# Optimization experiments

Hardware: AMD Instinct MI355X
Metric: run time of the kernel (lower is better)

Reference implementation:

```python
import jax, jax.numpy as jnp
import numpy as np

N, K, C, SP = 65536, 16, 64, 8
C8 = C // SP  # attn_nn output dim == C // share_planes == 8
E = N * K
EPS = 1e-5


def _bn(x, g, b):
    # BatchNorm1d in training mode: batch statistics over the row dim
    mu = x.mean(0)
    var = ((x - mu) ** 2).mean(0)
    return (x - mu) * jax.lax.rsqrt(var + EPS) * g + b


def _segment_softmax(a, seg, n):
    m = jax.ops.segment_max(a, seg, num_segments=n)
    e = jnp.exp(a - m[seg])
    s = jax.ops.segment_sum(e, seg, num_segments=n)
    return e / s[seg]


def setup_inputs() -> dict:
    key = jax.random.key(0)
    ks = jax.random.split(key, 12)

    def w(k, shape, fan_in):
        return jax.random.normal(k, shape, jnp.float32) / np.sqrt(fan_in).astype(np.float32)

    x = jax.random.normal(ks[0], (N, C), jnp.float32)
    pos = jax.random.uniform(ks[1], (N, 3), jnp.float32)
    src = jax.random.randint(ks[2], (E,), 0, N)          # knn neighbor ids
    dst = jnp.repeat(jnp.arange(N), K)                   # k neighbors per target node
    edge_index = jnp.stack([src, dst]).astype(jnp.int32)
    return dict(
        x=x, pos=pos, edge_index=edge_index,
        W_in=w(ks[3], (C, C), C), W_out=w(ks[4], (C, C), C),
        pos_w1=w(ks[5], (3, 3), 3), pos_b1=jnp.zeros(3, jnp.float32),
        pos_bn_g=jnp.ones(3, jnp.float32), pos_bn_b=jnp.zeros(3, jnp.float32),
        pos_w2=w(ks[6], (C, 3), 3), pos_b2=jnp.zeros(C, jnp.float32),
        attn_bn1_g=jnp.ones(C, jnp.float32), attn_bn1_b=jnp.zeros(C, jnp.float32),
        attn_w1=w(ks[7], (C8, C), C), attn_b1=jnp.zeros(C8, jnp.float32),
        attn_bn2_g=jnp.ones(C8, jnp.float32), attn_bn2_b=jnp.zeros(C8, jnp.float32),
        attn_w2=w(ks[8], (C8, C8), C8), attn_b2=jnp.zeros(C8, jnp.float32),
        lin_w=w(ks[9], (C, C), C), lin_b=jnp.zeros(C, jnp.float32),
        src_w=w(ks[10], (C, C), C), src_b=jnp.zeros(C, jnp.float32),
        dst_w=w(ks[11], (C, C), C), dst_b=jnp.zeros(C, jnp.float32),
        bn1_g=jnp.ones(C, jnp.float32), bn1_b=jnp.zeros(C, jnp.float32),
        bn2_g=jnp.ones(C, jnp.float32), bn2_b=jnp.zeros(C, jnp.float32),
        bn3_g=jnp.ones(C, jnp.float32), bn3_b=jnp.zeros(C, jnp.float32),
    )


def reference(x, pos, edge_index, W_in, W_out, pos_w1, pos_b1, pos_bn_g, pos_bn_b,
              pos_w2, pos_b2, attn_bn1_g, attn_bn1_b, attn_w1, attn_b1,
              attn_bn2_g, attn_bn2_b, attn_w2, attn_b2, lin_w, lin_b,
              src_w, src_b, dst_w, dst_b, bn1_g, bn1_b, bn2_g, bn2_b, bn3_g, bn3_b):
    src, dst = edge_index[0], edge_index[1]
    x_skip = x
    # lin_in + bn1 + relu
    h = jax.nn.relu(_bn(x @ W_in.T, bn1_g, bn1_b))

    # --- PointTransformerConv ---
    a_src = h @ src_w.T + src_b
    a_dst = h @ dst_w.T + dst_b
    hW = h @ lin_w.T + lin_b

    rel = pos[src] - pos[dst]              # pos_j - pos_i  [E,3]
    d = jax.nn.relu(_bn(rel @ pos_w1.T + pos_b1, pos_bn_g, pos_bn_b))
    delta = d @ pos_w2.T + pos_b2          # [E,C]

    a = a_src[src] - a_dst[dst] + delta    # alpha_j - alpha_i + delta  [E,C]
    # attn_nn: BN -> ReLU -> (Lin C->C8, BN, ReLU) -> Lin C8->C8
    a = jax.nn.relu(_bn(a, attn_bn1_g, attn_bn1_b))
    a = jax.nn.relu(_bn(a @ attn_w1.T + attn_b1, attn_bn2_g, attn_bn2_b))
    a = a @ attn_w2.T + attn_b2            # [E,C8]
    alpha = _segment_softmax(a, dst, N)    # softmax over each node's neighborhood

    # grouped weighting with share_planes: [E,SP,C8] * [E,1,C8]
    msg = (alpha[:, None, :] * (hW[src] + delta).reshape(E, SP, C8)).reshape(E, C)
    out = jax.ops.segment_sum(msg, dst, num_segments=N)  # aggr='add'

    h2 = jax.nn.relu(_bn(out, bn2_g, bn2_b))
    h3 = _bn(h2 @ W_out.T, bn3_g, bn3_b)
    return jax.nn.relu(h3 + x_skip)
```

## Files before the change

kernel.cpp:

```cpp
#include <hip/hip_runtime.h>
#include <cstddef>

constexpr int N_ = 65536;
constexpr int K_ = 16;
constexpr int E_ = N_ * K_;
constexpr int C_ = 64;
#define EPS_ 1e-5f
#define SW 68
#define INV_N (1.f / 65536.f)
#define INV_E (1.f / 1048576.f)
#define NSLOT 64

typedef unsigned int uint_t;
typedef float f32x4_t __attribute__((ext_vector_type(4)));
typedef short bf16x8_t __attribute__((ext_vector_type(8)));

__device__ __forceinline__ uint_t bf16_rne(float f) {
    uint_t u = __float_as_uint(f);
    return (u + 0x7fffu + ((u >> 16) & 1u)) >> 16;
}
__device__ __forceinline__ float bf16_lo(uint_t p) { return __uint_as_float(p << 16); }
__device__ __forceinline__ float bf16_hi(uint_t p) { return __uint_as_float(p & 0xffff0000u); }
__device__ __forceinline__ uint_t pk2(float a, float b) {
    return bf16_rne(a) | (bf16_rne(b) << 16);
}
__device__ __forceinline__ uint_t cvtpk(float lo, float hi) {
    uint_t r;
    asm("v_cvt_pk_bf16_f32 %0, %1, %2" : "=v"(r) : "v"(lo), "v"(hi));
    return r;
}

__device__ __forceinline__ void bn_ss(const float* __restrict__ s, int nchp, int c,
                                      float invM, const float* __restrict__ g,
                                      const float* __restrict__ b,
                                      float& sc, float& sh)
{
    float mean = s[c] * invM;
    float var  = fmaxf(s[nchp + c] * invM - mean * mean, 0.f);
    sc = g[c] * rsqrtf(var + EPS_);
    sh = b[c] - mean * sc;
}

__global__ void k_zero(float* __restrict__ p, int n)
{
    int i = blockIdx.x * 1024 + threadIdx.x;
    if (i < n) p[i] = 0.f;
}

__device__ __forceinline__ void stage_x(const float* __restrict__ in,
                                        const float* __restrict__ ss,
                                        float* __restrict__ Xs, int row0, int t)
{
#pragma unroll
    for (int it = 0; it < 4; ++it) {
        int m = t + 256 * it;
        int r = m >> 4, j = m & 15;
        float4 v = ((const float4*)in)[(size_t)(row0 + r) * 16 + j];
        if (ss) {
            float4 sc = ((const float4*)ss)[j];
            float4 sh = ((const float4*)(ss + 64))[j];
            v.x = fmaxf(fmaf(v.x, sc.x, sh.x), 0.f);
            v.y = fmaxf(fmaf(v.y, sc.y, sh.y), 0.f);
            v.z = fmaxf(fmaf(v.z, sc.z, sh.z), 0.f);
            v.w = fmaxf(fmaf(v.w, sc.w, sh.w), 0.f);
        }
        *(float4*)&Xs[r * SW + 4 * j] = v;
    }
}

__device__ __forceinline__ void stage_w(const float* __restrict__ W,
                                        float* __restrict__ Ws, int t)
{
#pragma unroll
    for (int it = 0; it < 4; ++it) {
        int m = t + 256 * it;
        int r = m >> 4, j = m & 15;
        *(float4*)&Ws[r * SW + 4 * j] = ((const float4*)W)[m];
    }
}

__device__ __forceinline__ void compute_tile(const float* __restrict__ Xs,
                                             const float* __restrict__ Ws,
                                             int tx, int ty, float acc[4][4])
{
#pragma unroll
    for (int r = 0; r < 4; ++r)
#pragma unroll
        for (int c = 0; c < 4; ++c) acc[r][c] = 0.f;
    for (int kc = 0; kc < 16; ++kc) {
        float4 xf[4], wf[4];
#pragma unroll
        for (int r = 0; r < 4; ++r)
            xf[r] = *(const float4*)&Xs[(tx + 16 * r) * SW + 4 * kc];
#pragma unroll
        for (int c = 0; c < 4; ++c)
            wf[c] = *(const float4*)&Ws[(ty + 16 * c) * SW + 4 * kc];
#pragma unroll
        for (int r = 0; r < 4; ++r)
#pragma unroll
            for (int c = 0; c < 4; ++c) {
                acc[r][c] = fmaf(xf[r].x, wf[c].x, acc[r][c]);
                acc[r][c] = fmaf(xf[r].y, wf[c].y, acc[r][c]);
                acc[r][c] = fmaf(xf[r].z, wf[c].z, acc[r][c]);
                acc[r][c] = fmaf(xf[r].w, wf[c].w, acc[r][c]);
            }
    }
}

__device__ __forceinline__ void write_tile(float* __restrict__ buf, int tx, int ty,
                                           const float acc[4][4],
                                           const float* __restrict__ bias,
                                           float* __restrict__ out, int row0, int t)
{
    __syncthreads();
#pragma unroll
    for (int r = 0; r < 4; ++r)
#pragma unroll
        for (int c = 0; c < 4; ++c)
            buf[(tx + 16 * r) * SW + ty + 16 * c] = acc[r][c];
    __syncthreads();
#pragma unroll
    for (int it = 0; it < 4; ++it) {
        int m = t + 256 * it;
        int r = m >> 4, j = m & 15;
        float4 v = *(const float4*)&buf[r * SW + 4 * j];
        if (bias) {
            float4 bv = ((const float4*)bias)[j];
            v.x += bv.x; v.y += bv.y; v.z += bv.z; v.w += bv.w;
        }
        ((float4*)out)[(size_t)(row0 + r) * 16 + j] = v;
    }
    __syncthreads();
}

__device__ __forceinline__ void write_tile_bf16(float* __restrict__ buf, int tx, int ty,
                                                const float acc[4][4],
                                                const float* __restrict__ bias,
                                                unsigned short* __restrict__ out,
                                                int row0, int t)
{
    __syncthreads();
#pragma unroll
    for (int r = 0; r < 4; ++r)
#pragma unroll
        for (int c = 0; c < 4; ++c)
            buf[(tx + 16 * r) * SW + ty + 16 * c] = acc[r][c];
    __syncthreads();
#pragma unroll
    for (int it = 0; it < 4; ++it) {
        int m = t + 256 * it;
        int r = m >> 4, j = m & 15;
        float4 v = *(const float4*)&buf[r * SW + 4 * j];
        if (bias) {
            float4 bv = ((const float4*)bias)[j];
            v.x += bv.x; v.y += bv.y; v.z += bv.z; v.w += bv.w;
        }
        uint2 o;
        o.x = bf16_rne(v.x) | (bf16_rne(v.y) << 16);
        o.y = bf16_rne(v.z) | (bf16_rne(v.w) << 16);
        ((uint2*)out)[(size_t)(row0 + r) * 16 + j] = o;
    }
    __syncthreads();
}

__global__ __launch_bounds__(256)
void k_gemm_tile(const float* __restrict__ in, const float* __restrict__ W,
                 const float* __restrict__ acc_in, const float* __restrict__ g_in,
                 const float* __restrict__ b_in, float invM_in,
                 float* __restrict__ out, float* __restrict__ acc_out)
{
    __shared__ float Xs[64 * SW];
    __shared__ float Ws[64 * SW];
    __shared__ float ssm[128];
    __shared__ float raws[128];
    int t = threadIdx.x, tx = t & 15, ty = t >> 4;
    int row0 = blockIdx.x * 64;
    if (acc_in) {
        if (t < 128) {
            float s = 0.f;
            for (int sl = 0; sl < NSLOT; ++sl) s += acc_in[sl * 128 + t];
            raws[t] = s;
        }
        __syncthreads();
        if (t < 64) {
            float scv, shv;
            bn_ss(raws, 64, t, invM_in, g_in, b_in, scv, shv);
            ssm[t] = scv; ssm[64 + t] = shv;
        }
    }
    __syncthreads();
    stage_x(in, acc_in ? ssm : nullptr, Xs, row0, t);
    stage_w(W, Ws, t);
    __syncthreads();
    float acc[4][4];
    compute_tile(Xs, Ws, tx, ty, acc);
    __syncthreads();
#pragma unroll
    for (int r = 0; r < 4; ++r)
#pragma unroll
        for (int c = 0; c < 4; ++c)
            Ws[(tx + 16 * r) * SW + ty + 16 * c] = acc[r][c];
    __syncthreads();
    float s0 = 0, s1 = 0, s2 = 0, s3 = 0, q0 = 0, q1 = 0, q2 = 0, q3 = 0;
#pragma unroll
    for (int it = 0; it < 4; ++it) {
        int m = t + 256 * it;
        int r = m >> 4, j = m & 15;
        float4 v = *(const float4*)&Ws[r * SW + 4 * j];
        ((float4*)out)[(size_t)(row0 + r) * 16 + j] = v;
        s0 += v.x; q0 = fmaf(v.x, v.x, q0);
        s1 += v.y; q1 = fmaf(v.y, v.y, q1);
        s2 += v.z; q2 = fmaf(v.z, v.z, q2);
        s3 += v.w; q3 = fmaf(v.w, v.w, q3);
    }
    float4* scr = (float4*)Xs;
    scr[t]       = make_float4(s0, s1, s2, s3);
    scr[256 + t] = make_float4(q0, q1, q2, q3);
    __syncthreads();
    if (t < 16) {
        float4 S = make_float4(0, 0, 0, 0), Q = make_float4(0, 0, 0, 0);
#pragma unroll
        for (int k = 0; k < 16; ++k) {
            float4 a = scr[k * 16 + t], b = scr[256 + k * 16 + t];
            S.x += a.x; S.y += a.y; S.z += a.z; S.w += a.w;
            Q.x += b.x; Q.y += b.y; Q.z += b.z; Q.w += b.w;
        }
        float* ao = acc_out + (blockIdx.x & (NSLOT - 1)) * 128;
        atomicAdd(&ao[4 * t + 0], S.x); atomicAdd(&ao[4 * t + 1], S.y);
        atomicAdd(&ao[4 * t + 2], S.z); atomicAdd(&ao[4 * t + 3], S.w);
        atomicAdd(&ao[64 + 4 * t + 0], Q.x); atomicAdd(&ao[64 + 4 * t + 1], Q.y);
        atomicAdd(&ao[64 + 4 * t + 2], Q.z); atomicAdd(&ao[64 + 4 * t + 3], Q.w);
    }
}

__global__ __launch_bounds__(256)
void k_gemm3_tile(const float* __restrict__ y, const float* __restrict__ acc1,
                  const float* __restrict__ g1, const float* __restrict__ b1,
                  const float* __restrict__ Wa, const float* __restrict__ ba,
                  const float* __restrict__ Wb, const float* __restrict__ bb,
                  const float* __restrict__ Wc, const float* __restrict__ bc,
                  unsigned short* __restrict__ oa16, float* __restrict__ ob,
                  unsigned short* __restrict__ oc16)
{
    __shared__ float Xs[64 * SW];
    __shared__ float Ws[64 * SW];
    __shared__ float ssm[128];
    __shared__ float raws[128];
    int t = threadIdx.x, tx = t & 15, ty = t >> 4;
    int row0 = blockIdx.x * 64;
    if (t < 128) {
        float s = 0.f;
        for (int sl = 0; sl < NSLOT; ++sl) s += acc1[sl * 128 + t];
        raws[t] = s;
    }
    __syncthreads();
    if (t < 64) {
        float scv, shv;
        bn_ss(raws, 64, t, INV_N, g1, b1, scv, shv);
        ssm[t] = scv; ssm[64 + t] = shv;
    }
    __syncthreads();
    stage_x(y, ssm, Xs, row0, t);
    stage_w(Wa, Ws, t);
    __syncthreads();
    float acc[4][4];
    compute_tile(Xs, Ws, tx, ty, acc);
    write_tile_bf16(Ws, tx, ty, acc, ba, oa16, row0, t);
    stage_w(Wb, Ws, t);
    __syncthreads();
    compute_tile(Xs, Ws, tx, ty, acc);
    write_tile(Ws, tx, ty, acc, bb, ob, row0, t);
    stage_w(Wc, Ws, t);
    __syncthreads();
    compute_tile(Xs, Ws, tx, ty, acc);
    write_tile_bf16(Ws, tx, ty, acc, bc, oc16, row0, t);
}

__global__ __launch_bounds__(256)
void k_pos_stats(const float* __restrict__ pos, const int* __restrict__ src,
                 const float* __restrict__ pw1, const float* __restrict__ pb1,
                 float* __restrict__ acc)
{
    float s0 = 0, s1 = 0, s2 = 0, q0 = 0, q1 = 0, q2 = 0;
    int tid = blockIdx.x * 256 + threadIdx.x;
    for (int e = tid; e < E_; e += 1024 * 256) {
        int si = src[e], di = e >> 4;
        float rx = pos[3 * si + 0] - pos[3 * di + 0];
        float ry = pos[3 * si + 1] - pos[3 * di + 1];
        float rz = pos[3 * si + 2] - pos[3 * di + 2];
        float u0 = fmaf(rx, pw1[0], fmaf(ry, pw1[1], fmaf(rz, pw1[2], pb1[0])));
        float u1 = fmaf(rx, pw1[3], fmaf(ry, pw1[4], fmaf(rz, pw1[5], pb1[1])));
        float u2 = fmaf(rx, pw1[6], fmaf(ry, pw1[7], fmaf(rz, pw1[8], pb1[2])));
        s0 += u0; q0 = fmaf(u0, u0, q0);
        s1 += u1; q1 = fmaf(u1, u1, q1);
        s2 += u2; q2 = fmaf(u2, u2, q2);
    }
#pragma unroll
    for (int m = 1; m < 64; m <<= 1) {
        s0 += __shfl_xor(s0, m, 64); s1 += __shfl_xor(s1, m, 64); s2 += __shfl_xor(s2, m, 64);
        q0 += __shfl_xor(q0, m, 64); q1 += __shfl_xor(q1, m, 64); q2 += __shfl_xor(q2, m, 64);
    }
    __shared__ float red[4][8];
    int wv = threadIdx.x >> 6, ln = threadIdx.x & 63;
    if (ln == 0) {
        red[wv][0] = s0; red[wv][1] = s1; red[wv][2] = s2; red[wv][3] = 0.f;
        red[wv][4] = q0; red[wv][5] = q1; red[wv][6] = q2; red[wv][7] = 0.f;
    }
    __syncthreads();
    if (threadIdx.x < 8)
        atomicAdd(&acc[(blockIdx.x & (NSLOT - 1)) * 32 + threadIdx.x],
                  red[0][threadIdx.x] + red[1][threadIdx.x] + red[2][threadIdx.x] + red[3][threadIdx.x]);
}

__global__ __launch_bounds__(256)
void k_abn1_stats(const float* __restrict__ pos, const int* __restrict__ src,
                  const unsigned short* __restrict__ asrc16,
                  const float* __restrict__ adst,
                  const float* __restrict__ pw1, const float* __restrict__ pb1,
                  const float* __restrict__ accpos, const float* __restrict__ pbg,
                  const float* __restrict__ pbb, const float* __restrict__ pw2,
                  const float* __restrict__ pb2, float* __restrict__ acc_a1)
{
    __shared__ float rawP[8];
    int t = threadIdx.x;
    int l = t & 15, g = t >> 4, wv = t >> 6;
    int c0 = 4 * l;
    if (t < 8) {
        float s = 0.f;
        for (int sl = 0; sl < NSLOT; ++sl) s += accpos[sl * 32 + t];
        rawP[t] = s;
    }
    __syncthreads();
    float ps0, ph0, ps1, ph1, ps2, ph2;
    bn_ss(rawP, 4, 0, INV_E, pbg, pbb, ps0, ph0);
    bn_ss(rawP, 4, 1, INV_E, pbg, pbb, ps1, ph1);
    bn_ss(rawP, 4, 2, INV_E, pbg, pbb, ps2, ph2);
    float4 p0 = *(const float4*)(pw2 + 12 * l);
    float4 p1 = *(const float4*)(pw2 + 12 * l + 4);
    float4 p2 = *(const float4*)(pw2 + 12 * l + 8);
    float4 pb = *(const float4*)(pb2 + c0);
    float sa0 = 0, sa1 = 0, sa2 = 0, sa3 = 0;
    float qa0 = 0, qa1 = 0, qa2 = 0, qa3 = 0;
#pragma unroll
    for (int nn = 0; nn < 2; ++nn) {
        int n = blockIdx.x * 32 + nn * 16 + g;
        float4 dv = *(const float4*)(adst + (size_t)n * 64 + c0);
        float pnx = pos[3 * n + 0], pny = pos[3 * n + 1], pnz = pos[3 * n + 2];
        int si_l = src[n * 16 + l];
        float rx = pos[3 * si_l + 0] - pnx;
        float ry = pos[3 * si_l + 1] - pny;
        float rz = pos[3 * si_l + 2] - pnz;
        float u0 = fmaf(rx, pw1[0], fmaf(ry, pw1[1], fmaf(rz, pw1[2], pb1[0])));
        float u1 = fmaf(rx, pw1[3], fmaf(ry, pw1[4], fmaf(rz, pw1[5], pb1[1])));
        float u2 = fmaf(rx, pw1[6], fmaf(ry, pw1[7], fmaf(rz, pw1[8], pb1[2])));
        float dl0 = fmaxf(fmaf(u0, ps0, ph0), 0.f);
        float dl1 = fmaxf(fmaf(u1, ps1, ph1), 0.f);
        float dl2 = fmaxf(fmaf(u2, ps2, ph2), 0.f);
        for (int k = 0; k < 16; ++k) {
            int si = __shfl(si_l, k, 16);
            float d0 = __shfl(dl0, k, 16);
            float d1 = __shfl(dl1, k, 16);
            float d2 = __shfl(dl2, k, 16);
            uint2 raw = ((const uint2*)asrc16)[(size_t)si * 16 + l];
            float avx = bf16_lo(raw.x), avy = bf16_hi(raw.x);
            float avz = bf16_lo(raw.y), avw = bf16_hi(raw.y);
            float del0 = fmaf(d0, p0.x, fmaf(d1, p0.y, fmaf(d2, p0.z, pb.x)));
            float del1 = fmaf(d0, p0.w, fmaf(d1, p1.x, fmaf(d2, p1.y, pb.y)));
            float del2 = fmaf(d0, p1.z, fmaf(d1, p1.w, fmaf(d2, p2.x, pb.z)));
            float del3 = fmaf(d0, p2.y, fmaf(d1, p2.z, fmaf(d2, p2.w, pb.w)));
            float a0 = avx - dv.x + del0;
            float a1 = avy - dv.y + del1;
            float a2 = avz - dv.z + del2;
            float a3 = avw - dv.w + del3;
            sa0 += a0; qa0 = fmaf(a0, a0, qa0);
            sa1 += a1; qa1 = fmaf(a1, a1, qa1);
            sa2 += a2; qa2 = fmaf(a2, a2, qa2);
            sa3 += a3; qa3 = fmaf(a3, a3, qa3);
        }
    }
#pragma unroll
    for (int m = 16; m <= 32; m <<= 1) {
        sa0 += __shfl_xor(sa0, m, 64); sa1 += __shfl_xor(sa1, m, 64);
        sa2 += __shfl_xor(sa2, m, 64); sa3 += __shfl_xor(sa3, m, 64);
        qa0 += __shfl_xor(qa0, m, 64); qa1 += __shfl_xor(qa1, m, 64);
        qa2 += __shfl_xor(qa2, m, 64); qa3 += __shfl_xor(qa3, m, 64);
    }
    __shared__ float red[4][128];
    if ((t & 63) < 16) {
        red[wv][c0 + 0] = sa0; red[wv][c0 + 1] = sa1;
        red[wv][c0 + 2] = sa2; red[wv][c0 + 3] = sa3;
        red[wv][64 + c0 + 0] = qa0; red[wv][64 + c0 + 1] = qa1;
        red[wv][64 + c0 + 2] = qa2; red[wv][64 + c0 + 3] = qa3;
    }
    __syncthreads();
    if (t < 128)
        atomicAdd(&acc_a1[(blockIdx.x & (NSLOT - 1)) * 128 + t],
                  red[0][t] + red[1][t] + red[2][t] + red[3][t]);
}

__global__ __launch_bounds__(256)
void k_edge_t1(const float* __restrict__ pos, const int* __restrict__ src,
               const unsigned short* __restrict__ asrc16,
               const float* __restrict__ adst,
               const float* __restrict__ pw1, const float* __restrict__ pb1,
               const float* __restrict__ accpos, const float* __restrict__ pbg,
               const float* __restrict__ pbb, const float* __restrict__ pw2,
               const float* __restrict__ pb2, const float* __restrict__ acc_a1,
               const float* __restrict__ a1g, const float* __restrict__ a1b,
               const float* __restrict__ aw1, const float* __restrict__ ab1,
               float* __restrict__ t1, float* __restrict__ acc_a2)
{
    __shared__ uint2 an_lds[4096];
    float* shf = (float*)an_lds;
    char*  anb = (char*)an_lds;
    int t = threadIdx.x;
    int l = t & 15, g = t >> 4, wv = t >> 6;
    int L = t & 63;
    int c0 = 4 * l;
    if (t < 128) {
        float s = 0.f;
        for (int sl = 0; sl < NSLOT; ++sl) s += acc_a1[sl * 128 + t];
        shf[t] = s;
    } else if (t < 136) {
        int i = t - 128;
        float s = 0.f;
        for (int sl = 0; sl < NSLOT; ++sl) s += accpos[sl * 32 + i];
        shf[128 + i] = s;
    }
    __syncthreads();
    float ps0, ph0, ps1, ph1, ps2, ph2;
    bn_ss(shf + 128, 4, 0, INV_E, pbg, pbb, ps0, ph0);
    bn_ss(shf + 128, 4, 1, INV_E, pbg, pbb, ps1, ph1);
    bn_ss(shf + 128, 4, 2, INV_E, pbg, pbb, ps2, ph2);
    float scx, shx, scy, shy, scz, shz, scw, shw;
    bn_ss(shf, 64, c0 + 0, INV_E, a1g, a1b, scx, shx);
    bn_ss(shf, 64, c0 + 1, INV_E, a1g, a1b, scy, shy);
    bn_ss(shf, 64, c0 + 2, INV_E, a1g, a1b, scz, shz);
    bn_ss(shf, 64, c0 + 3, INV_E, a1g, a1b, scw, shw);
    float4 p0 = *(const float4*)(pw2 + 12 * l);
    float4 p1 = *(const float4*)(pw2 + 12 * l + 4);
    float4 p2 = *(const float4*)(pw2 + 12 * l + 8);
    float4 pb = *(const float4*)(pb2 + c0);
    float Pa0 = p0.x * scx, Pa1 = p0.y * scx, Pa2 = p0.z * scx;
    float Pb0 = p0.w * scy, Pb1 = p1.x * scy, Pb2 = p1.y * scy;
    float Pc0 = p1.z * scz, Pc1 = p1.w * scz, Pc2 = p2.x * scz;
    float Pd0 = p2.y * scw, Pd1 = p2.z * scw, Pd2 = p2.w * scw;
    float qb0 = fmaf(pb.x, scx, shx);
    float qb1 = fmaf(pb.y, scy, shy);
    float qb2 = fmaf(pb.z, scz, shz);
    float qb3 = fmaf(pb.w, scw, shw);
    int col = L & 15, kb = L >> 4;
    uint4 bf0 = make_uint4(0u, 0u, 0u, 0u);
    uint4 bf1 = make_uint4(0u, 0u, 0u, 0u);
    float biasc = 0.f;
    if (col < 8) {
        const float* wr = aw1 + col * 64 + kb * 8;
        bf0 = make_uint4(pk2(wr[0], wr[1]), pk2(wr[2], wr[3]),
                         pk2(wr[4], wr[5]), pk2(wr[6], wr[7]));
        const float* wr2 = wr + 32;
        bf1 = make_uint4(pk2(wr2[0], wr2[1]), pk2(wr2[2], wr2[3]),
                         pk2(wr2[4], wr2[5]), pk2(wr2[6], wr2[7]));
        biasc = ab1[col];
    }
    int ar = col;
    int aoff0 = ar * 128 + ((kb * 16) ^ ((ar & 7) << 4));
    int aoff1 = ar * 128 + ((64 + kb * 16) ^ ((ar & 7) << 4));
    __syncthreads();
    float se = 0.f, sq = 0.f;
#pragma unroll
    for (int nn = 0; nn < 2; ++nn) {
        int n = blockIdx.x * 32 + nn * 16 + g;
        float4 dv = *(const float4*)(adst + (size_t)n * 64 + c0);
        float q0n = fmaf(-dv.x, scx, qb0);
        float q1n = fmaf(-dv.y, scy, qb1);
        float q2n = fmaf(-dv.z, scz, qb2);
        float q3n = fmaf(-dv.w, scw, qb3);
        float pnx = pos[3 * n + 0], pny = pos[3 * n + 1], pnz = pos[3 * n + 2];
        int si_l = src[n * 16 + l];
        float rx = pos[3 * si_l + 0] - pnx;
        float ry = pos[3 * si_l + 1] - pny;
        float rz = pos[3 * si_l + 2] - pnz;
        float u0 = fmaf(rx, pw1[0], fmaf(ry, pw1[1], fmaf(rz, pw1[2], pb1[0])));
        float u1 = fmaf(rx, pw1[3], fmaf(ry, pw1[4], fmaf(rz, pw1[5], pb1[1])));
        float u2 = fmaf(rx, pw1[6], fmaf(ry, pw1[7], fmaf(rz, pw1[8], pb1[2])));
        float dl0 = fmaxf(fmaf(u0, ps0, ph0), 0.f);
        float dl1 = fmaxf(fmaf(u1, ps1, ph1), 0.f);
        float dl2 = fmaxf(fmaf(u2, ps2, ph2), 0.f);
#pragma unroll
        for (int k = 0; k < 16; ++k) {
            int si = __shfl(si_l, k, 16);
            float d0 = __shfl(dl0, k, 16);
            float d1 = __shfl(dl1, k, 16);
            float d2 = __shfl(dl2, k, 16);
            uint2 raw = ((const uint2*)asrc16)[(size_t)si * 16 + l];
            float avx = bf16_lo(raw.x), avy = bf16_hi(raw.x);
            float avz = bf16_lo(raw.y), avw = bf16_hi(raw.y);
            float de0 = fmaf(d0, Pa0, fmaf(d1, Pa1, fmaf(d2, Pa2, q0n)));
            float de1 = fmaf(d0, Pb0, fmaf(d1, Pb1, fmaf(d2, Pb2, q1n)));
            float de2 = fmaf(d0, Pc0, fmaf(d1, Pc1, fmaf(d2, Pc2, q2n)));
            float de3 = fmaf(d0, Pd0, fmaf(d1, Pd1, fmaf(d2, Pd2, q3n)));
            float an0 = fmaxf(fmaf(avx, scx, de0), 0.f);
            float an1 = fmaxf(fmaf(avy, scy, de1), 0.f);
            float an2 = fmaxf(fmaf(avz, scz, de2), 0.f);
            float an3 = fmaxf(fmaf(avw, scw, de3), 0.f);
            int woff = g * 2048 + k * 128 + ((8 * l) ^ ((k & 7) << 4));
            *(uint2*)(anb + woff) = make_uint2(cvtpk(an0, an1), cvtpk(an2, an3));
        }
#pragma unroll
        for (int tt = 0; tt < 4; ++tt) {
            int g2 = (wv << 2) + tt;
            int tb = g2 * 2048;
            uint4 a0 = *(const uint4*)(anb + tb + aoff0);
            uint4 a1v = *(const uint4*)(anb + tb + aoff1);
            f32x4_t acc = {0.f, 0.f, 0.f, 0.f};
            acc = __builtin_amdgcn_mfma_f32_16x16x32_bf16(
                      *(const bf16x8_t*)&a0, *(const bf16x8_t*)&bf0, acc, 0, 0, 0);
            acc = __builtin_amdgcn_mfma_f32_16x16x32_bf16(
                      *(const bf16x8_t*)&a1v, *(const bf16x8_t*)&bf1, acc, 0, 0, 0);
            if (col < 8) {
                int n2 = blockIdx.x * 32 + nn * 16 + g2;
                float* op = t1 + (size_t)(n2 * 16 + kb * 4) * 8 + col;
#pragma unroll
                for (int j = 0; j < 4; ++j) {
                    float v = acc[j] + biasc;
                    op[j * 8] = v;
                    se += v; sq = fmaf(v, v, sq);
                }
            }
        }
    }
    se += __shfl_xor(se, 16, 64); sq += __shfl_xor(sq, 16, 64);
    se += __shfl_xor(se, 32, 64); sq += __shfl_xor(sq, 32, 64);
    __syncthreads();
    if (L < 8) { shf[wv * 16 + col] = se; shf[wv * 16 + 8 + col] = sq; }
    __syncthreads();
    if (t < 16)
        atomicAdd(&acc_a2[(blockIdx.x & (NSLOT - 1)) * 32 + t],
                  shf[t] + shf[16 + t] + shf[32 + t] + shf[48 + t]);
}

__global__ __launch_bounds__(256)
void k_node_aggr(const float* __restrict__ pos, const int* __restrict__ src,
                 const float* __restrict__ t1, const float* __restrict__ acc_a2,
                 const float* __restrict__ a2g, const float* __restrict__ a2b,
                 const float* __restrict__ aw2, const float* __restrict__ ab2,
                 const unsigned short* __restrict__ hw16,
                 const float* __restrict__ accpos, const float* __restrict__ pbg,
                 const float* __restrict__ pbb,
                 const float* __restrict__ pw1, const float* __restrict__ pb1,
                 const float* __restrict__ pw2, const float* __restrict__ pb2,
                 float* __restrict__ out, float* __restrict__ acc_bn2)
{
    __shared__ float alds[16][196];
    __shared__ float ssm2[16];
    __shared__ float rawA2[16];
    __shared__ float rawP[8];
    int t = threadIdx.x, l = t & 15, g = t >> 4;
    int c0 = 4 * l;
    if (t < 16) {
        float s = 0.f;
        for (int sl = 0; sl < NSLOT; ++sl) s += acc_a2[sl * 32 + t];
        rawA2[t] = s;
    } else if (t < 24) {
        int i = t - 16;
        float s = 0.f;
        for (int sl = 0; sl < NSLOT; ++sl) s += accpos[sl * 32 + i];
        rawP[i] = s;
    }
    __syncthreads();
    if (t < 8) {
        float scv, shv;
        bn_ss(rawA2, 8, t, INV_E, a2g, a2b, scv, shv);
        ssm2[t] = scv; ssm2[8 + t] = shv;
    }
    __syncthreads();
    float ps0, ph0, ps1, ph1, ps2, ph2;
    bn_ss(rawP, 4, 0, INV_E, pbg, pbb, ps0, ph0);
    bn_ss(rawP, 4, 1, INV_E, pbg, pbb, ps1, ph1);
    bn_ss(rawP, 4, 2, INV_E, pbg, pbb, ps2, ph2);
    float4 p0 = *(const float4*)(pw2 + 12 * l);
    float4 p1 = *(const float4*)(pw2 + 12 * l + 4);
    float4 p2 = *(const float4*)(pw2 + 12 * l + 8);
    float4 pb = *(const float4*)(pb2 + c0);
    int alof = (l & 1) * 4;
    int n = blockIdx.x * 16 + g;
    int e = n * 16 + l;
    const float4* t4 = (const float4*)(t1 + (size_t)e * 8);
    float4 ta = t4[0], tb = t4[1];
    float tv[8] = {ta.x, ta.y, ta.z, ta.w, tb.x, tb.y, tb.z, tb.w};
    float tn[8];
#pragma unroll
    for (int j = 0; j < 8; ++j)
        tn[j] = fmaxf(fmaf(tv[j], ssm2[j], ssm2[8 + j]), 0.f);
    float al[8];
#pragma unroll
    for (int j = 0; j < 8; ++j) {
        float acc = ab2[j];
#pragma unroll
        for (int i = 0; i < 8; ++i) acc = fmaf(tn[i], aw2[j * 8 + i], acc);
        float m = acc;
#pragma unroll
        for (int msk = 1; msk < 16; msk <<= 1) m = fmaxf(m, __shfl_xor(m, msk, 64));
        float ex = __expf(acc - m);
        float sm = ex;
#pragma unroll
        for (int msk = 1; msk < 16; msk <<= 1) sm += __shfl_xor(sm, msk, 64);
        al[j] = ex / sm;
    }
    *(float4*)&alds[g][l * 12]     = make_float4(al[0], al[1], al[2], al[3]);
    *(float4*)&alds[g][l * 12 + 4] = make_float4(al[4], al[5], al[6], al[7]);
    int silane = src[e];
    float pnx = pos[3 * n + 0], pny = pos[3 * n + 1], pnz = pos[3 * n + 2];
    float rx = pos[3 * silane + 0] - pnx;
    float ry = pos[3 * silane + 1] - pny;
    float rz = pos[3 * silane + 2] - pnz;
    float u0 = fmaf(rx, pw1[0], fmaf(ry, pw1[1], fmaf(rz, pw1[2], pb1[0])));
    float u1 = fmaf(rx, pw1[3], fmaf(ry, pw1[4], fmaf(rz, pw1[5], pb1[1])));
    float u2 = fmaf(rx, pw1[6], fmaf(ry, pw1[7], fmaf(rz, pw1[8], pb1[2])));
    float dl0 = fmaxf(fmaf(u0, ps0, ph0), 0.f);
    float dl1 = fmaxf(fmaf(u1, ps1, ph1), 0.f);
    float dl2 = fmaxf(fmaf(u2, ps2, ph2), 0.f);
    float a0 = 0.f, a1 = 0.f, a2 = 0.f, a3 = 0.f;
#pragma unroll 4
    for (int k = 0; k < 16; ++k) {
        int sk = __shfl(silane, k, 16);
        float d0 = __shfl(dl0, k, 16);
        float d1 = __shfl(dl1, k, 16);
        float d2 = __shfl(dl2, k, 16);
        uint2 raw = ((const uint2*)hw16)[(size_t)sk * 16 + l];
        float hvx = bf16_lo(raw.x), hvy = bf16_hi(raw.x);
        float hvz = bf16_lo(raw.y), hvw = bf16_hi(raw.y);
        float4 alv = *(const float4*)&alds[g][k * 12 + alof];
        float del0 = fmaf(d0, p0.x, fmaf(d1, p0.y, fmaf(d2, p0.z, pb.x)));
        float del1 = fmaf(d0, p0.w, fmaf(d1, p1.x, fmaf(d2, p1.y, pb.y)));
        float del2 = fmaf(d0, p1.z, fmaf(d1, p1.w, fmaf(d2, p2.x, pb.z)));
        float del3 = fmaf(d0, p2.y, fmaf(d1, p2.z, fmaf(d2, p2.w, pb.w)));
        a0 = fmaf(alv.x, hvx + del0, a0);
        a1 = fmaf(alv.y, hvy + del1, a1);
        a2 = fmaf(alv.z, hvz + del2, a2);
        a3 = fmaf(alv.w, hvw + del3, a3);
    }
    *(float4*)(out + (size_t)n * 64 + c0) = make_float4(a0, a1, a2, a3);
    __syncthreads();
    float4* scr = (float4*)&alds[0][0];
    scr[g * 16 + l]       = make_float4(a0, a1, a2, a3);
    scr[256 + g * 16 + l] = make_float4(a0 * a0, a1 * a1, a2 * a2, a3 * a3);
    __syncthreads();
    if (t < 16) {
        float4 S = make_float4(0, 0, 0, 0), Q = make_float4(0, 0, 0, 0);
#pragma unroll
        for (int k = 0; k < 16; ++k) {
            float4 a = scr[k * 16 + t], b = scr[256 + k * 16 + t];
            S.x += a.x; S.y += a.y; S.z += a.z; S.w += a.w;
            Q.x += b.x; Q.y += b.y; Q.z += b.z; Q.w += b.w;
        }
        float* ao = acc_bn2 + (blockIdx.x & (NSLOT - 1)) * 128;
        atomicAdd(&ao[4 * t + 0], S.x); atomicAdd(&ao[4 * t + 1], S.y);
        atomicAdd(&ao[4 * t + 2], S.z); atomicAdd(&ao[4 * t + 3], S.w);
        atomicAdd(&ao[64 + 4 * t + 0], Q.x); atomicAdd(&ao[64 + 4 * t + 1], Q.y);
        atomicAdd(&ao[64 + 4 * t + 2], Q.z); atomicAdd(&ao[64 + 4 * t + 3], Q.w);
    }
}

__global__ __launch_bounds__(256)
void k_final(const float* __restrict__ y3, const float* __restrict__ acc3,
             const float* __restrict__ g3, const float* __restrict__ b3,
             const float* __restrict__ x, float* __restrict__ out)
{
    __shared__ float raws[128];
    __shared__ float ssl[128];
    int t = threadIdx.x;
    if (t < 128) {
        float s = 0.f;
        for (int sl = 0; sl < NSLOT; ++sl) s += acc3[sl * 128 + t];
        raws[t] = s;
    }
    __syncthreads();
    if (t < 64) {
        float scv, shv;
        bn_ss(raws, 64, t, INV_N, g3, b3, scv, shv);
        ssl[t] = scv; ssl[64 + t] = shv;
    }
    __syncthreads();
    int i = blockIdx.x * 256 + t;
    int c4 = i & 15;
    float4 sc = *(const float4*)&ssl[4 * c4];
    float4 sh = *(const float4*)&ssl[64 + 4 * c4];
    float4 v  = ((const float4*)y3)[i];
    float4 xs = ((const float4*)x)[i];
    float4 o;
    o.x = fmaxf(fmaf(v.x, sc.x, sh.x) + xs.x, 0.f);
    o.y = fmaxf(fmaf(v.y, sc.y, sh.y) + xs.y, 0.f);
    o.z = fmaxf(fmaf(v.z, sc.z, sh.z) + xs.z, 0.f);
    o.w = fmaxf(fmaf(v.w, sc.w, sh.w) + xs.w, 0.f);
    ((float4*)out)[i] = o;
}

extern "C" void kernel_launch(void* const* d_in, const int* in_sizes, int n_in,
                              void* d_out, int out_size, void* d_ws, size_t ws_size,
                              hipStream_t stream)
{
    const float* x    = (const float*)d_in[0];
    const float* pos  = (const float*)d_in[1];
    const int*   src  = (const int*)d_in[2];
    const float* W_in = (const float*)d_in[3];
    const float* W_out= (const float*)d_in[4];
    const float* pw1  = (const float*)d_in[5];
    const float* pb1  = (const float*)d_in[6];
    const float* pbg  = (const float*)d_in[7];
    const float* pbb  = (const float*)d_in[8];
    const float* pw2  = (const float*)d_in[9];
    const float* pb2  = (const float*)d_in[10];
    const float* a1g  = (const float*)d_in[11];
    const float* a1b  = (const float*)d_in[12];
    const float* aw1  = (const float*)d_in[13];
    const float* ab1  = (const float*)d_in[14];
    const float* a2g  = (const float*)d_in[15];
    const float* a2b  = (const float*)d_in[16];
    const float* aw2  = (const float*)d_in[17];
    const float* ab2  = (const float*)d_in[18];
    const float* linw = (const float*)d_in[19];
    const float* linb = (const float*)d_in[20];
    const float* srcw = (const float*)d_in[21];
    const float* srcb = (const float*)d_in[22];
    const float* dstw = (const float*)d_in[23];
    const float* dstb = (const float*)d_in[24];
    const float* bn1g = (const float*)d_in[25];
    const float* bn1b = (const float*)d_in[26];
    const float* bn2g = (const float*)d_in[27];
    const float* bn2b = (const float*)d_in[28];
    const float* bn3g = (const float*)d_in[29];
    const float* bn3b = (const float*)d_in[30];
    float* outp = (float*)d_out;

    float* ws = (float*)d_ws;
    const size_t NC = (size_t)N_ * C_;
    float* buf_y     = ws;
    float* buf_adst  = ws + NC;
    unsigned short* asrc16 = (unsigned short*)(ws + 2 * NC);
    unsigned short* hw16   = (unsigned short*)(ws + 2 * NC + NC / 2);
    float* buf_t1    = ws + 3 * NC;
    float* accb      = ws + 3 * NC + (size_t)E_ * 8;
    float* acc_bn1 = accb;
    float* acc_pos = accb + 64 * 128;
    float* acc_a1  = acc_pos + 64 * 32;
    float* acc_a2  = acc_a1 + 64 * 128;
    float* acc_bn2 = acc_a2 + 64 * 32;
    float* acc_bn3 = acc_bn2 + 64 * 128;
    const int ACC_TOTAL = 64 * (128 + 32 + 128 + 32 + 128 + 128);
    float* buf_out = buf_adst;

    k_zero<<<(ACC_TOTAL + 1023) / 1024, 1024, 0, stream>>>(accb, ACC_TOTAL);
    k_gemm_tile<<<1024, 256, 0, stream>>>(x, W_in, nullptr, nullptr, nullptr, 0.f,
                                          buf_y, acc_bn1);
    k_gemm3_tile<<<1024, 256, 0, stream>>>(buf_y, acc_bn1, bn1g, bn1b,
                                           srcw, srcb, dstw, dstb, linw, linb,
                                           asrc16, buf_adst, hw16);
    k_pos_stats<<<1024, 256, 0, stream>>>(pos, src, pw1, pb1, acc_pos);
    k_abn1_stats<<<2048, 256, 0, stream>>>(pos, src, asrc16, buf_adst,
                                           pw1, pb1, acc_pos, pbg, pbb,
                                           pw2, pb2, acc_a1);
    k_edge_t1<<<2048, 256, 0, stream>>>(pos, src, asrc16, buf_adst,
                                        pw1, pb1, acc_pos, pbg, pbb, pw2, pb2,
                                        acc_a1, a1g, a1b, aw1, ab1,
                                        buf_t1, acc_a2);
    k_node_aggr<<<4096, 256, 0, stream>>>(pos, src, buf_t1, acc_a2, a2g, a2b,
                                          aw2, ab2, hw16, acc_pos, pbg, pbb,
                                          pw1, pb1, pw2, pb2, buf_out, acc_bn2);
    k_gemm_tile<<<1024, 256, 0, stream>>>(buf_out, W_out, acc_bn2, bn2g, bn2b, INV_N,
                                          buf_y, acc_bn3);
    k_final<<<(N_ * C_ / 4) / 256, 256, 0, stream>>>(buf_y, acc_bn3, bn3g, bn3b, x, outp);

    (void)in_sizes; (void)n_in; (void)out_size; (void)ws_size;
}
```

Before: 308.1 us.

## Replace FP32 FMA node GEMMs with split-bf16 MFMA (3-pass) in tile kernels

The per-node 64x64 GEMM kernels (k_gemm_tile and k_gemm3_tile) now split inputs and weights into high and low bf16 parts and compute with 16x16x32 bf16 MFMA instructions using three products (hh, lh, hl), in place of scalar FP32 FMAs. The shared-memory layout changes to packed bf16 tiles, and the result is restaged through LDS for coalesced stores. This is meant to offload the node GEMMs to matrix cores. It adds split conversions, slightly lower precision than FP32, and extra synchronizations. These node-level GEMMs are a small share of a pipeline dominated by edge work.

```diff
diff --git a/kernel.cpp b/kernel.cpp
--- a/kernel.cpp
+++ b/kernel.cpp
@@ -30,6 +30,13 @@
     return r;
 }
 
+__device__ __forceinline__ void split4(float4 v, uint2& h, uint2& l) {
+    h.x = cvtpk(v.x, v.y); h.y = cvtpk(v.z, v.w);
+    float r0 = v.x - bf16_lo(h.x), r1 = v.y - bf16_hi(h.x);
+    float r2 = v.z - bf16_lo(h.y), r3 = v.w - bf16_hi(h.y);
+    l.x = cvtpk(r0, r1); l.y = cvtpk(r2, r3);
+}
+
 __device__ __forceinline__ void bn_ss(const float* __restrict__ s, int nchp, int c,
                                       float invM, const float* __restrict__ g,
                                       const float* __restrict__ b,
@@ -47,9 +54,13 @@
     if (i < n) p[i] = 0.f;
 }
 
-__device__ __forceinline__ void stage_x(const float* __restrict__ in,
-                                        const float* __restrict__ ss,
-                                        float* __restrict__ Xs, int row0, int t)
+#define TS 36
+
+__device__ __forceinline__ void stage_x_split(const float* __restrict__ in,
+                                              const float* __restrict__ ss,
+                                              uint_t* __restrict__ Xh,
+                                              uint_t* __restrict__ Xl,
+                                              int row0, int t)
 {
 #pragma unroll
     for (int it = 0; it < 4; ++it) {
@@ -64,103 +75,71 @@
             v.z = fmaxf(fmaf(v.z, sc.z, sh.z), 0.f);
             v.w = fmaxf(fmaf(v.w, sc.w, sh.w), 0.f);
         }
-        *(float4*)&Xs[r * SW + 4 * j] = v;
-    }
-}
-
-__device__ __forceinline__ void stage_w(const float* __restrict__ W,
-                                        float* __restrict__ Ws, int t)
+        uint2 h, l; split4(v, h, l);
+        *(uint2*)&Xh[r * TS + 2 * j] = h;
+        *(uint2*)&Xl[r * TS + 2 * j] = l;
+    }
+}
+
+__device__ __forceinline__ void stage_w_split(const float* __restrict__ W,
+                                              uint_t* __restrict__ Wh,
+                                              uint_t* __restrict__ Wl, int t)
 {
 #pragma unroll
     for (int it = 0; it < 4; ++it) {
         int m = t + 256 * it;
         int r = m >> 4, j = m & 15;
-        *(float4*)&Ws[r * SW + 4 * j] = ((const float4*)W)[m];
-    }
-}
-
-__device__ __forceinline__ void compute_tile(const float* __restrict__ Xs,
-                                             const float* __restrict__ Ws,
-                                             int tx, int ty, float acc[4][4])
-{
-#pragma unroll
-    for (int r = 0; r < 4; ++r)
-#pragma unroll
-        for (int c = 0; c < 4; ++c) acc[r][c] = 0.f;
-    for (int kc = 0; kc < 16; ++kc) {
-        float4 xf[4], wf[4];
-#pragma unroll
-        for (int r = 0; r < 4; ++r)
-            xf[r] = *(const float4*)&Xs[(tx + 16 * r) * SW + 4 * kc];
-#pragma unroll
-        for (int c = 0; c < 4; ++c)
-            wf[c] = *(const float4*)&Ws[(ty + 16 * c) * SW + 4 * kc];
-#pragma unroll
-        for (int r = 0; r < 4; ++r)
-#pragma unroll
-            for (int c = 0; c < 4; ++c) {
-                acc[r][c] = fmaf(xf[r].x, wf[c].x, acc[r][c]);
-                acc[r][c] = fmaf(xf[r].y, wf[c].y, acc[r][c]);
-                acc[r][c] = fmaf(xf[r].z, wf[c].z, acc[r][c]);
-                acc[r][c] = fmaf(xf[r].w, wf[c].w, acc[r][c]);
-            }
-    }
-}
-
-__device__ __forceinline__ void write_tile(float* __restrict__ buf, int tx, int ty,
-                                           const float acc[4][4],
-                                           const float* __restrict__ bias,
-                                           float* __restrict__ out, int row0, int t)
-{
-    __syncthreads();
-#pragma unroll
-    for (int r = 0; r < 4; ++r)
-#pragma unroll
-        for (int c = 0; c < 4; ++c)
-            buf[(tx + 16 * r) * SW + ty + 16 * c] = acc[r][c];
-    __syncthreads();
-#pragma unroll
-    for (int it = 0; it < 4; ++it) {
-        int m = t + 256 * it;
-        int r = m >> 4, j = m & 15;
-        float4 v = *(const float4*)&buf[r * SW + 4 * j];
-        if (bias) {
-            float4 bv = ((const float4*)bias)[j];
-            v.x += bv.x; v.y += bv.y; v.z += bv.z; v.w += bv.w;
-        }
-        ((float4*)out)[(size_t)(row0 + r) * 16 + j] = v;
-    }
-    __syncthreads();
-}
-
-__device__ __forceinline__ void write_tile_bf16(float* __restrict__ buf, int tx, int ty,
-                                                const float acc[4][4],
-                                                const float* __restrict__ bias,
-                                                unsigned short* __restrict__ out,
-                                                int row0, int t)
-{
-    __syncthreads();
-#pragma unroll
-    for (int r = 0; r < 4; ++r)
-#pragma unroll
-        for (int c = 0; c < 4; ++c)
-            buf[(tx + 16 * r) * SW + ty + 16 * c] = acc[r][c];
-    __syncthreads();
-#pragma unroll
-    for (int it = 0; it < 4; ++it) {
-        int m = t + 256 * it;
-        int r = m >> 4, j = m & 15;
-        float4 v = *(const float4*)&buf[r * SW + 4 * j];
-        if (bias) {
-            float4 bv = ((const float4*)bias)[j];
-            v.x += bv.x; v.y += bv.y; v.z += bv.z; v.w += bv.w;
-        }
-        uint2 o;
-        o.x = bf16_rne(v.x) | (bf16_rne(v.y) << 16);
-        o.y = bf16_rne(v.z) | (bf16_rne(v.w) << 16);
-        ((uint2*)out)[(size_t)(row0 + r) * 16 + j] = o;
-    }
-    __syncthreads();
+        float4 v = ((const float4*)W)[m];
+        uint2 h, l; split4(v, h, l);
+        *(uint2*)&Wh[r * TS + 2 * j] = h;
+        *(uint2*)&Wl[r * TS + 2 * j] = l;
+    }
+}
+
+struct AFrag { uint4 h0, h1, l0, l1; };
+
+__device__ __forceinline__ AFrag load_afrag(const uint_t* __restrict__ Xh,
+                                            const uint_t* __restrict__ Xl,
+                                            int L, int wv)
+{
+    int cl = L & 15, kb = L >> 4;
+    int o = (16 * wv + cl) * TS + kb * 4;
+    AFrag a;
+    a.h0 = *(const uint4*)&Xh[o]; a.h1 = *(const uint4*)&Xh[o + 16];
+    a.l0 = *(const uint4*)&Xl[o]; a.l1 = *(const uint4*)&Xl[o + 16];
+    return a;
+}
+
+#define MF(A, B, C) __builtin_amdgcn_mfma_f32_16x16x32_bf16( \
+        *(const bf16x8_t*)&(A), *(const bf16x8_t*)&(B), (C), 0, 0, 0)
+
+__device__ __forceinline__ void mfma_tile(const AFrag& af,
+                                          const uint_t* __restrict__ Wh,
+                                          const uint_t* __restrict__ Wl,
+                                          int L, f32x4_t acc[4])
+{
+    int cl = L & 15, kb = L >> 4;
+#pragma unroll
+    for (int ct = 0; ct < 4; ++ct) {
+        int o = (ct * 16 + cl) * TS + kb * 4;
+        uint4 Bh0 = *(const uint4*)&Wh[o], Bh1 = *(const uint4*)&Wh[o + 16];
+        uint4 Bl0 = *(const uint4*)&Wl[o], Bl1 = *(const uint4*)&Wl[o + 16];
+        f32x4_t a = {0.f, 0.f, 0.f, 0.f};
+        a = MF(af.h0, Bh0, a); a = MF(af.l0, Bh0, a); a = MF(af.h0, Bl0, a);
+        a = MF(af.h1, Bh1, a); a = MF(af.l1, Bh1, a); a = MF(af.h1, Bl1, a);
+        acc[ct] = a;
+    }
+}
+
+__device__ __forceinline__ void ytile_store(float* __restrict__ ybuf, int L, int wv,
+                                            const f32x4_t acc[4])
+{
+    int cl = L & 15, kb = L >> 4;
+#pragma unroll
+    for (int ct = 0; ct < 4; ++ct)
+#pragma unroll
+        for (int j = 0; j < 4; ++j)
+            ybuf[(16 * wv + kb * 4 + j) * SW + ct * 16 + cl] = acc[ct][j];
 }
 
 __global__ __launch_bounds__(256)
@@ -169,11 +148,14 @@
                  const float* __restrict__ b_in, float invM_in,
                  float* __restrict__ out, float* __restrict__ acc_out)
 {
-    __shared__ float Xs[64 * SW];
-    __shared__ float Ws[64 * SW];
+    __shared__ __align__(16) uint_t shb[4 * 64 * TS];
     __shared__ float ssm[128];
     __shared__ float raws[128];
-    int t = threadIdx.x, tx = t & 15, ty = t >> 4;
+    uint_t* Xh = shb;           uint_t* Xl = shb + 64 * TS;
+    uint_t* Wh = shb + 2 * 64 * TS; uint_t* Wl = shb + 3 * 64 * TS;
+    float* ybuf = (float*)shb;
+    float4* scr = (float4*)((float*)shb + 4352);
+    int t = threadIdx.x, L = t & 63, wv = t >> 6;
     int row0 = blockIdx.x * 64;
     if (acc_in) {
         if (t < 128) {
@@ -189,31 +171,27 @@
         }
     }
     __syncthreads();
-    stage_x(in, acc_in ? ssm : nullptr, Xs, row0, t);
-    stage_w(W, Ws, t);
-    __syncthreads();
-    float acc[4][4];
-    compute_tile(Xs, Ws, tx, ty, acc);
-    __syncthreads();
-#pragma unroll
-    for (int r = 0; r < 4; ++r)
-#pragma unroll
-        for (int c = 0; c < 4; ++c)
-            Ws[(tx + 16 * r) * SW + ty + 16 * c] = acc[r][c];
+    stage_x_split(in, acc_in ? ssm : nullptr, Xh, Xl, row0, t);
+    stage_w_split(W, Wh, Wl, t);
+    __syncthreads();
+    AFrag af = load_afrag(Xh, Xl, L, wv);
+    f32x4_t acc[4];
+    mfma_tile(af, Wh, Wl, L, acc);
+    __syncthreads();
+    ytile_store(ybuf, L, wv, acc);
     __syncthreads();
     float s0 = 0, s1 = 0, s2 = 0, s3 = 0, q0 = 0, q1 = 0, q2 = 0, q3 = 0;
 #pragma unroll
     for (int it = 0; it < 4; ++it) {
         int m = t + 256 * it;
         int r = m >> 4, j = m & 15;
-        float4 v = *(const float4*)&Ws[r * SW + 4 * j];
+        float4 v = *(const float4*)&ybuf[r * SW + 4 * j];
         ((float4*)out)[(size_t)(row0 + r) * 16 + j] = v;
         s0 += v.x; q0 = fmaf(v.x, v.x, q0);
         s1 += v.y; q1 = fmaf(v.y, v.y, q1);
         s2 += v.z; q2 = fmaf(v.z, v.z, q2);
         s3 += v.w; q3 = fmaf(v.w, v.w, q3);
     }
-    float4* scr = (float4*)Xs;
     scr[t]       = make_float4(s0, s1, s2, s3);
     scr[256 + t] = make_float4(q0, q1, q2, q3);
     __syncthreads();
@@ -242,11 +220,13 @@
                   unsigned short* __restrict__ oa16, float* __restrict__ ob,
                   unsigned short* __restrict__ oc16)
 {
-    __shared__ float Xs[64 * SW];
-    __shared__ float Ws[64 * SW];
+    __shared__ __align__(16) uint_t shb[4 * 64 * TS];
     __shared__ float ssm[128];
     __shared__ float raws[128];
-    int t = threadIdx.x, tx = t & 15, ty = t >> 4;
+    uint_t* Xh = shb;           uint_t* Xl = shb + 64 * TS;
+    uint_t* Wh = shb + 2 * 64 * TS; uint_t* Wl = shb + 3 * 64 * TS;
+    float* ybuf = (float*)shb;
+    int t = threadIdx.x, L = t & 63, wv = t >> 6;
     int row0 = blockIdx.x * 64;
     if (t < 128) {
         float s = 0.f;
@@ -260,20 +240,60 @@
         ssm[t] = scv; ssm[64 + t] = shv;
     }
     __syncthreads();
-    stage_x(y, ssm, Xs, row0, t);
-    stage_w(Wa, Ws, t);
-    __syncthreads();
-    float acc[4][4];
-    compute_tile(Xs, Ws, tx, ty, acc);
-    write_tile_bf16(Ws, tx, ty, acc, ba, oa16, row0, t);
-    stage_w(Wb, Ws, t);
-    __syncthreads();
-    compute_tile(Xs, Ws, tx, ty, acc);
-    write_tile(Ws, tx, ty, acc, bb, ob, row0, t);
-    stage_w(Wc, Ws, t);
-    __syncthreads();
-    compute_tile(Xs, Ws, tx, ty, acc);
-    write_tile_bf16(Ws, tx, ty, acc, bc, oc16, row0, t);
+    stage_x_split(y, ssm, Xh, Xl, row0, t);
+    stage_w_split(Wa, Wh, Wl, t);
+    __syncthreads();
+    AFrag af = load_afrag(Xh, Xl, L, wv);
+    f32x4_t acc[4];
+    mfma_tile(af, Wh, Wl, L, acc);
+    __syncthreads();
+    ytile_store(ybuf, L, wv, acc);
+    __syncthreads();
+#pragma unroll
+    for (int it = 0; it < 4; ++it) {
+        int m = t + 256 * it;
+        int r = m >> 4, j = m & 15;
+        float4 v = *(const float4*)&ybuf[r * SW + 4 * j];
+        float4 bv = ((const float4*)ba)[j];
+        uint2 o;
+        o.x = pk2(v.x + bv.x, v.y + bv.y);
+        o.y = pk2(v.z + bv.z, v.w + bv.w);
+        ((uint2*)oa16)[(size_t)(row0 + r) * 16 + j] = o;
+    }
+    __syncthreads();
+    stage_w_split(Wb, Wh, Wl, t);
+    __syncthreads();
+    mfma_tile(af, Wh, Wl, L, acc);
+    __syncthreads();
+    ytile_store(ybuf, L, wv, acc);
+    __syncthreads();
+#pragma unroll
+    for (int it = 0; it < 4; ++it) {
+        int m = t + 256 * it;
+        int r = m >> 4, j = m & 15;
+        float4 v = *(const float4*)&ybuf[r * SW + 4 * j];
+        float4 bv = ((const float4*)bb)[j];
+        v.x += bv.x; v.y += bv.y; v.z += bv.z; v.w += bv.w;
+        ((float4*)ob)[(size_t)(row0 + r) * 16 + j] = v;
+    }
+    __syncthreads();
+    stage_w_split(Wc, Wh, Wl, t);
+    __syncthreads();
+    mfma_tile(af, Wh, Wl, L, acc);
+    __syncthreads();
+    ytile_store(ybuf, L, wv, acc);
+    __syncthreads();
+#pragma unroll
+    for (int it = 0; it < 4; ++it) {
+        int m = t + 256 * it;
+        int r = m >> 4, j = m & 15;
+        float4 v = *(const float4*)&ybuf[r * SW + 4 * j];
+        float4 bv = ((const float4*)bc)[j];
+        uint2 o;
+        o.x = pk2(v.x + bv.x, v.y + bv.y);
+        o.y = pk2(v.z + bv.z, v.w + bv.w);
+        ((uint2*)oc16)[(size_t)(row0 + r) * 16 + j] = o;
+    }
 }
 
 __global__ __launch_bounds__(256)
```

Result: faster. 287.6 us (-6.7%).
